# Optimization experiments

Hardware: AMD Instinct MI355X
Metric: run time of the kernel (lower is better)

## Reference

```python
import jax, jax.numpy as jnp
import numpy as np

DIM = 2048
N_HEADS = 16
HEAD_DIM = DIM // N_HEADS
ROPE_BASE = 10000


def l2norm(x, axis=-1, eps=1e-12):
    n = jnp.sqrt(jnp.sum(x * x, axis=axis, keepdims=True))
    return x / jnp.maximum(n, eps)


def rope_tables(T, dim, base, dtype):
    theta = 1.0 / (base ** (jnp.arange(0, dim, 2, dtype=dtype) / dim))  # [dim/2]
    ang = jnp.arange(T, dtype=dtype)[:, None] * theta[None, :]          # [T, dim/2]
    return jnp.sin(ang), jnp.cos(ang)


def apply_rope(x, sin, cos):
    # x: [B, H, T, D]; sin/cos: [T, D/2] (half-split convention, not interleaved)
    half = x.shape[-1] // 2
    xr, xi = x[..., :half], x[..., half:]
    yr = xr * cos - xi * sin
    yi = xr * sin + xi * cos
    return jnp.concatenate([yr, yi], axis=-1)


def setup_inputs() -> dict:
    key = jax.random.key(0)
    ks = jax.random.split(key, 5)
    B, T = 1, 2048
    x = jax.random.normal(ks[0], (B, T, DIM), dtype=jnp.float32)
    wq = jax.random.normal(ks[1], (DIM, DIM), dtype=jnp.float32) * 0.02
    wk = jax.random.normal(ks[2], (DIM, DIM), dtype=jnp.float32) * 0.02
    wv = jax.random.normal(ks[3], (DIM, DIM), dtype=jnp.float32) * 0.02
    wo = jax.random.normal(ks[4], (DIM, DIM), dtype=jnp.float32) * 0.02
    sqk = jnp.ones((N_HEADS, 1, HEAD_DIM), dtype=jnp.float32) * (1.0 / DIM ** 0.5)
    return {"x": x, "wq": wq, "wk": wk, "wv": wv, "wo": wo, "sqk": sqk}


def reference(x, wq, wk, wv, wo, sqk):
    B, T, C = x.shape
    H, D = N_HEADS, HEAD_DIM
    restore = C ** 0.5  # restore_scale_sqk = sqkinit / sqkscale
    actual_sqk = sqk * restore  # [H, 1, D]

    def proj(w):
        return jnp.einsum('btc,oc->bto', x, w).reshape(B, T, H, D).transpose(0, 2, 1, 3)

    q = proj(wq)  # [B, H, T, D]
    new_k = proj(wk)
    new_v = proj(wv)

    sin, cos = rope_tables(T, D, ROPE_BASE, x.dtype)
    q = apply_rope(q, sin, cos) * actual_sqk
    k = apply_rope(new_k, sin, cos) * actual_sqk

    # NOTE: original uses scale=head_dim**0.5 (multiplies by sqrt(D))
    scores = jnp.einsum('bhqd,bhkd->bhqk', q, k) * (D ** 0.5)
    mask = jnp.tril(jnp.ones((T, T), dtype=bool))
    scores = jnp.where(mask, scores, jnp.finfo(scores.dtype).min)
    attn = jax.nn.softmax(scores, axis=-1)
    out = jnp.einsum('bhqk,bhkd->bhqd', attn, new_v)  # [B, H, T, D]
    out = out.transpose(0, 2, 1, 3).reshape(B, T, C)
    out = jnp.einsum('btc,oc->bto', out, wo)
    return (l2norm(out), (new_k, new_v))
```

## Files before the change

kernel.cpp:

```cpp
#include <hip/hip_runtime.h>

typedef __bf16 bf16x8 __attribute__((ext_vector_type(8)));
typedef float f32x4 __attribute__((ext_vector_type(4)));
typedef unsigned short us4 __attribute__((ext_vector_type(4)));

constexpr int TT = 2048;
constexpr int CC = 2048;
constexpr int HH = 16;
constexpr int DD = 128;

__device__ __forceinline__ unsigned short f2bf(float f) {
  unsigned u = __builtin_bit_cast(unsigned, f);
  u += 0x7FFFu + ((u >> 16) & 1u);
  return (unsigned short)(u >> 16);
}
__device__ __forceinline__ float bf2f(unsigned short b) {
  unsigned u = ((unsigned)b) << 16;
  return __builtin_bit_cast(float, u);
}

__device__ __forceinline__ void gld_lds16(const unsigned short* g, unsigned short* l) {
  __builtin_amdgcn_global_load_lds(
      (const __attribute__((address_space(1))) unsigned int*)g,
      (__attribute__((address_space(3))) unsigned int*)l,
      16, 0, 0);
}

__device__ __forceinline__ int soff(int qt) {
  int g = qt >> 2, rem = qt & 3;
  return (g + 1) * (2 * g + rem);
}

__global__ __launch_bounds__(256) void k_f32_to_bf16(
    const float* __restrict__ src, unsigned short* __restrict__ dst, int n8) {
  int i = blockIdx.x * 256 + threadIdx.x;
  if (i >= n8) return;
  const float4* s = (const float4*)src;
  float4 a = s[2 * i], b = s[2 * i + 1];
  us4 lo = { f2bf(a.x), f2bf(a.y), f2bf(a.z), f2bf(a.w) };
  us4 hi = { f2bf(b.x), f2bf(b.y), f2bf(b.z), f2bf(b.w) };
  us4* d = (us4*)dst;
  d[2 * i] = lo;
  d[2 * i + 1] = hi;
}

template <int MODE>
__global__ __launch_bounds__(512, 2) void k_gemm256(
    const unsigned short* __restrict__ A, const unsigned short* __restrict__ B,
    int N, int K, int kspan,
    float* __restrict__ out0, float* __restrict__ out1,
    float* __restrict__ out2, float* __restrict__ out3) {
  __shared__ alignas(16) unsigned short As[2][2][128 * 64];
  __shared__ alignas(16) unsigned short Bs[2][2][128 * 64];
  const int tid = threadIdx.x;
  const int m0 = blockIdx.y * 256, n0 = blockIdx.x * 256;
  const int kbeg = blockIdx.z * kspan;
  const int NT = kspan >> 6;
  const int wid = tid >> 6, lane = tid & 63;
  const int wr = wid >> 2, wc = wid & 3;
  const int lr = lane & 15, lg = lane >> 4;
  const int swz = lr & 7;
  const int bh = wc >> 1;
  const int brow0 = (wc & 1) * 64;

  const int sr0 = tid >> 3, sc0 = tid & 7;
  const unsigned short* Ab = A + kbeg;
  const unsigned short* Bb = B + kbeg;

  auto stageA = [&](int buf, int half, int koff) {
#pragma unroll
    for (int j = 0; j < 2; ++j) {
      const int r = sr0 + j * 64;
      gld_lds16(Ab + (size_t)(m0 + half * 128 + r) * K + koff + ((sc0 ^ (r & 7)) * 8),
                &As[buf][half][(tid + j * 512) * 8]);
    }
  };
  auto stageB = [&](int buf, int half, int koff) {
#pragma unroll
    for (int j = 0; j < 2; ++j) {
      const int r = sr0 + j * 64;
      gld_lds16(Bb + (size_t)(n0 + half * 128 + r) * K + koff + ((sc0 ^ (r & 7)) * 8),
                &Bs[buf][half][(tid + j * 512) * 8]);
    }
  };

  f32x4 acc[8][4] = {};

  stageA(0, 0, 0); stageA(0, 1, 0); stageB(0, 0, 0); stageB(0, 1, 0);
  if (NT > 1) {
    stageA(1, 0, 64); stageA(1, 1, 64); stageB(1, 0, 64); stageB(1, 1, 64);
    asm volatile("s_waitcnt vmcnt(8)" ::: "memory");
  } else {
    asm volatile("s_waitcnt vmcnt(0)" ::: "memory");
  }
  __builtin_amdgcn_sched_barrier(0);
  __builtin_amdgcn_s_barrier();

  for (int t = 0; t < NT; ++t) {
    const int cur = t & 1;
    const int kN2 = (t + 2) * 64;
    const bool pf = (t + 2) < NT;
    bf16x8 alo[4][2], ahi[4][2], ba[2][2], bb[2][2];

#pragma unroll
    for (int im = 0; im < 4; ++im)
#pragma unroll
      for (int kk = 0; kk < 2; ++kk)
        alo[im][kk] = *(const bf16x8*)(&As[cur][wr][(im * 16 + lr) * 64 + (((kk * 4 + lg) ^ swz) * 8)]);
#pragma unroll
    for (int in = 0; in < 2; ++in)
#pragma unroll
      for (int kk = 0; kk < 2; ++kk)
        ba[in][kk] = *(const bf16x8*)(&Bs[cur][bh][(brow0 + in * 16 + lr) * 64 + (((kk * 4 + lg) ^ swz) * 8)]);
#pragma unroll
    for (int in = 0; in < 2; ++in)
#pragma unroll
      for (int kk = 0; kk < 2; ++kk)
        bb[in][kk] = *(const bf16x8*)(&Bs[cur][bh][(brow0 + (2 + in) * 16 + lr) * 64 + (((kk * 4 + lg) ^ swz) * 8)]);
    asm volatile("s_waitcnt lgkmcnt(4)" ::: "memory");
    __builtin_amdgcn_sched_barrier(0);

    __builtin_amdgcn_s_setprio(1);
#pragma unroll
    for (int im = 0; im < 4; ++im)
#pragma unroll
      for (int in = 0; in < 2; ++in)
#pragma unroll
        for (int kk = 0; kk < 2; ++kk)
          acc[im][in] = __builtin_amdgcn_mfma_f32_16x16x32_bf16(alo[im][kk], ba[in][kk], acc[im][in], 0, 0, 0);
    __builtin_amdgcn_s_setprio(0);
    asm volatile("s_waitcnt lgkmcnt(0)" ::: "memory");
    __builtin_amdgcn_sched_barrier(0);

    __builtin_amdgcn_s_setprio(1);
#pragma unroll
    for (int im = 0; im < 4; ++im)
#pragma unroll
      for (int in = 0; in < 2; ++in)
#pragma unroll
        for (int kk = 0; kk < 2; ++kk)
          acc[im][2 + in] = __builtin_amdgcn_mfma_f32_16x16x32_bf16(alo[im][kk], bb[in][kk], acc[im][2 + in], 0, 0, 0);
    __builtin_amdgcn_s_setprio(0);
    __builtin_amdgcn_sched_barrier(0);

#pragma unroll
    for (int im = 0; im < 4; ++im)
#pragma unroll
      for (int kk = 0; kk < 2; ++kk)
        ahi[im][kk] = *(const bf16x8*)(&As[cur][wr][((4 + im) * 16 + lr) * 64 + (((kk * 4 + lg) ^ swz) * 8)]);

    __builtin_amdgcn_s_barrier();
    if (pf) { stageB(cur, 0, kN2); stageB(cur, 1, kN2); }
    asm volatile("s_waitcnt lgkmcnt(0)" ::: "memory");
    __builtin_amdgcn_sched_barrier(0);

    __builtin_amdgcn_s_setprio(1);
#pragma unroll
    for (int im = 0; im < 4; ++im)
#pragma unroll
      for (int in = 0; in < 2; ++in)
#pragma unroll
        for (int kk = 0; kk < 2; ++kk)
          acc[4 + im][2 + in] = __builtin_amdgcn_mfma_f32_16x16x32_bf16(ahi[im][kk], bb[in][kk], acc[4 + im][2 + in], 0, 0, 0);
    __builtin_amdgcn_s_setprio(0);
    __builtin_amdgcn_sched_barrier(0);

    __builtin_amdgcn_s_barrier();
    if (pf) { stageA(cur, 0, kN2); stageA(cur, 1, kN2); }

    __builtin_amdgcn_s_setprio(1);
#pragma unroll
    for (int im = 0; im < 4; ++im)
#pragma unroll
      for (int in = 0; in < 2; ++in)
#pragma unroll
        for (int kk = 0; kk < 2; ++kk)
          acc[4 + im][in] = __builtin_amdgcn_mfma_f32_16x16x32_bf16(ahi[im][kk], ba[in][kk], acc[4 + im][in], 0, 0, 0);
    __builtin_amdgcn_s_setprio(0);
    __builtin_amdgcn_sched_barrier(0);
    if (pf) {
      asm volatile("s_waitcnt vmcnt(8)" ::: "memory");
    } else {
      asm volatile("s_waitcnt vmcnt(0)" ::: "memory");
    }
    __builtin_amdgcn_sched_barrier(0);
    __builtin_amdgcn_s_barrier();
  }

  float* dst = out0;
  if (MODE == 1) {
    int z = blockIdx.z;
    dst = (z == 0) ? out0 : (z == 1) ? out1 : (z == 2) ? out2 : out3;
  }
#pragma unroll
  for (int mf = 0; mf < 8; ++mf) {
    const int row = m0 + wr * 128 + mf * 16 + lg * 4;
#pragma unroll
    for (int nf = 0; nf < 4; ++nf) {
      const int col = n0 + wc * 64 + nf * 16 + lr;
#pragma unroll
      for (int r = 0; r < 4; ++r) {
        float v = acc[mf][nf][r];
        int rr = row + r;
        if (MODE == 0) {
          if (col < 2048) {
            out0[(size_t)rr * 2048 + col] = v;
          } else if (col < 4096) {
            int c = col - 2048;
            out1[(size_t)(c >> 7) * (TT * DD) + (size_t)rr * DD + (c & 127)] = v;
          } else {
            int c = col - 4096;
            out2[(size_t)(c >> 7) * (TT * DD) + (size_t)rr * DD + (c & 127)] = v;
          }
        } else {
          dst[(size_t)rr * N + col] = v;
        }
      }
    }
  }
}

__global__ __launch_bounds__(256) void k_rope(
    const float* __restrict__ Qf, const float* __restrict__ Kraw,
    const float* __restrict__ sqk,
    unsigned short* __restrict__ qb, unsigned short* __restrict__ kb) {
  const int t = blockIdx.x;
  for (int i = threadIdx.x; i < HH * 64; i += 256) {
    int h = i >> 6, dp = i & 63;
    float theta = expf(-(float)dp * 0.14391156831212787f);
    float ang = (float)t * theta;
    float sn, cs;
    sincosf(ang, &sn, &cs);
    float qr = Qf[(size_t)t * CC + h * DD + dp];
    float qi = Qf[(size_t)t * CC + h * DD + dp + 64];
    const float* kp = Kraw + (size_t)h * TT * DD + (size_t)t * DD;
    float kr = kp[dp], ki = kp[dp + 64];
    float sr = sqk[h * DD + dp];
    float si = sqk[h * DD + dp + 64];
    float qsr = sr * 512.0f, qsi = si * 512.0f;
    float ksr = sr * 45.25483399593904f, ksi = si * 45.25483399593904f;
    unsigned short* qo = qb + ((size_t)h * TT + t) * DD;
    unsigned short* ko = kb + ((size_t)h * TT + t) * DD;
    qo[dp]      = f2bf((qr * cs - qi * sn) * qsr);
    qo[dp + 64] = f2bf((qr * sn + qi * cs) * qsi);
    ko[dp]      = f2bf((kr * cs - ki * sn) * ksr);
    ko[dp + 64] = f2bf((kr * sn + ki * cs) * ksi);
  }
}

__global__ __launch_bounds__(256) void k_vt(
    const float* __restrict__ Vraw, unsigned short* __restrict__ vt) {
  const int h = blockIdx.z;
  const int t0 = blockIdx.x * 64, d0 = blockIdx.y * 64;
  __shared__ unsigned short tile[64][65];
  const float* vp = Vraw + (size_t)h * TT * DD;
  for (int i = threadIdx.x; i < 4096; i += 256) {
    int r = i >> 6, c = i & 63;
    tile[r][c] = f2bf(vp[(size_t)(t0 + r) * DD + d0 + c]);
  }
  __syncthreads();
  unsigned short* op = vt + (size_t)h * DD * TT;
  for (int i = threadIdx.x; i < 4096; i += 256) {
    int dr = i >> 6, tc = i & 63;
    op[(size_t)(d0 + dr) * TT + t0 + tc] = tile[tc][dr];
  }
}

__global__ __launch_bounds__(512) void k_attn_split(
    const unsigned short* __restrict__ qb, const unsigned short* __restrict__ kb,
    const unsigned short* __restrict__ vt,
    unsigned short* __restrict__ po, float* __restrict__ marr, float* __restrict__ larr) {
  const int qt = blockIdx.x, h = blockIdx.y, s = blockIdx.z;
  if (4 * s > qt) return;
  const int slot = h * 40 + soff(qt) + s;
  const int kbeg = 512 * s;
  const int kend = min(kbeg + 512, 128 * qt + 128);
  const int ntiles = (kend - kbeg) >> 6;
  const int tid = threadIdx.x;
  const int wid = tid >> 6, lane = tid & 63;
  const int lr = lane & 15, lg = lane >> 4;
  const int q0 = qt * 128 + wid * 16;

  __shared__ alignas(16) unsigned short Ks[64 * 128];
  __shared__ alignas(16) unsigned short Vs[128 * 64];
  __shared__ alignas(16) unsigned short P[8][16][72];

  const unsigned short* qh = qb + (size_t)h * TT * DD;
  const unsigned short* kh = kb + (size_t)h * TT * DD;
  const unsigned short* vh = vt + (size_t)h * DD * TT;

  bf16x8 qf[4];
#pragma unroll
  for (int c = 0; c < 4; ++c)
    qf[c] = *(const bf16x8*)(qh + (size_t)(q0 + lr) * DD + c * 32 + lg * 8);

  f32x4 acc[8] = {};
  float mrow[4] = {-3e38f, -3e38f, -3e38f, -3e38f};
  float lsum[4] = {0.f, 0.f, 0.f, 0.f};

  for (int kt = 0; kt < ntiles; ++kt) {
    const int k0 = kbeg + kt * 64;
#pragma unroll
    for (int half = 0; half < 2; ++half) {
      int ch = tid + half * 512;
      int r = ch >> 4, c4 = ch & 15;
      gld_lds16(kh + (size_t)(k0 + r) * DD + ((c4 ^ (r & 7)) * 8), Ks + ch * 8);
    }
#pragma unroll
    for (int half = 0; half < 2; ++half) {
      int ch = tid + half * 512;
      int d = ch >> 3, c8 = ch & 7;
      gld_lds16(vh + (size_t)d * TT + k0 + ((c8 ^ (d & 7)) * 8), Vs + ch * 8);
    }
    __syncthreads();

    if (k0 <= q0 + 15) {
      f32x4 sv[4] = {};
#pragma unroll
      for (int ktile = 0; ktile < 4; ++ktile) {
        const int row = ktile * 16 + lr;
#pragma unroll
        for (int c = 0; c < 4; ++c) {
          int chn = (c * 4 + lg) ^ (lr & 7);
          bf16x8 kf = *(const bf16x8*)(Ks + row * 128 + chn * 8);
          sv[ktile] = __builtin_amdgcn_mfma_f32_16x16x32_bf16(qf[c], kf, sv[ktile], 0, 0, 0);
        }
      }
      if (k0 + 63 > q0) {
#pragma unroll
        for (int ktile = 0; ktile < 4; ++ktile)
#pragma unroll
          for (int r = 0; r < 4; ++r) {
            int key = k0 + ktile * 16 + lr;
            int qrow = q0 + lg * 4 + r;
            if (key > qrow) sv[ktile][r] = -1e30f;
          }
      }
      float pmax[4];
#pragma unroll
      for (int r = 0; r < 4; ++r)
        pmax[r] = fmaxf(fmaxf(sv[0][r], sv[1][r]), fmaxf(sv[2][r], sv[3][r]));
#pragma unroll
      for (int msk = 1; msk <= 8; msk <<= 1)
#pragma unroll
        for (int r = 0; r < 4; ++r) pmax[r] = fmaxf(pmax[r], __shfl_xor(pmax[r], msk));
      float p[4][4], ps[4], scl[4];
#pragma unroll
      for (int r = 0; r < 4; ++r) {
        float mn = fmaxf(mrow[r], pmax[r]);
        scl[r] = __expf(mrow[r] - mn);
        mrow[r] = mn;
        ps[r] = 0.f;
#pragma unroll
        for (int ktile = 0; ktile < 4; ++ktile) {
          p[ktile][r] = __expf(sv[ktile][r] - mn);
          ps[r] += p[ktile][r];
        }
      }
#pragma unroll
      for (int msk = 1; msk <= 8; msk <<= 1)
#pragma unroll
        for (int r = 0; r < 4; ++r) ps[r] += __shfl_xor(ps[r], msk);
#pragma unroll
      for (int r = 0; r < 4; ++r) lsum[r] = lsum[r] * scl[r] + ps[r];
#pragma unroll
      for (int n = 0; n < 8; ++n)
#pragma unroll
        for (int r = 0; r < 4; ++r) acc[n][r] *= scl[r];
#pragma unroll
      for (int ktile = 0; ktile < 4; ++ktile)
#pragma unroll
        for (int r = 0; r < 4; ++r)
          P[wid][lg * 4 + r][ktile * 16 + lr] = f2bf(p[ktile][r]);
      asm volatile("s_waitcnt lgkmcnt(0)" ::: "memory");
      __builtin_amdgcn_sched_barrier(0);
      bf16x8 pf[2];
#pragma unroll
      for (int ks = 0; ks < 2; ++ks)
        pf[ks] = *(const bf16x8*)(&P[wid][lr][ks * 32 + lg * 8]);
#pragma unroll
      for (int n = 0; n < 8; ++n) {
        const int row = n * 16 + lr;
#pragma unroll
        for (int ks = 0; ks < 2; ++ks) {
          int chn = (ks * 4 + lg) ^ (lr & 7);
          bf16x8 vf = *(const bf16x8*)(Vs + row * 64 + chn * 8);
          acc[n] = __builtin_amdgcn_mfma_f32_16x16x32_bf16(pf[ks], vf, acc[n], 0, 0, 0);
        }
      }
    }
    __syncthreads();
  }

  unsigned short* pob = po + (size_t)slot * (128 * DD);
#pragma unroll
  for (int n = 0; n < 8; ++n)
#pragma unroll
    for (int r = 0; r < 4; ++r) {
      int row = wid * 16 + lg * 4 + r;
      pob[(size_t)row * DD + n * 16 + lr] = f2bf(acc[n][r]);
    }
  if (lr == 0) {
#pragma unroll
    for (int r = 0; r < 4; ++r) {
      int row = wid * 16 + lg * 4 + r;
      marr[(size_t)slot * 128 + row] = mrow[r];
      larr[(size_t)slot * 128 + row] = lsum[r];
    }
  }
}

__global__ __launch_bounds__(256) void k_attn_reduce(
    const unsigned short* __restrict__ po, const float* __restrict__ marr,
    const float* __restrict__ larr, unsigned short* __restrict__ ob) {
  const int qt = blockIdx.x, h = blockIdx.y;
  const int ns = (qt >> 2) + 1;
  const int sb = h * 40 + soff(qt);
  const int tid = threadIdx.x;
  const int row = tid >> 1, d0 = (tid & 1) * 64;
  float mstar = -3e38f;
  for (int s = 0; s < ns; ++s) mstar = fmaxf(mstar, marr[(size_t)(sb + s) * 128 + row]);
  float w[4];
  float ltot = 0.f;
  for (int s = 0; s < ns; ++s) {
    w[s] = __expf(marr[(size_t)(sb + s) * 128 + row] - mstar);
    ltot += w[s] * larr[(size_t)(sb + s) * 128 + row];
  }
  float inv = 1.0f / ltot;
  float o[64] = {};
  for (int s = 0; s < ns; ++s) {
    const bf16x8* pp = (const bf16x8*)(po + (size_t)(sb + s) * (128 * DD) + (size_t)row * DD + d0);
    float ws = w[s];
#pragma unroll
    for (int j = 0; j < 8; ++j) {
      bf16x8 v = pp[j];
#pragma unroll
      for (int e = 0; e < 8; ++e) o[j * 8 + e] += ws * (float)v[e];
    }
  }
  unsigned short* op = ob + (size_t)(qt * 128 + row) * CC + h * DD + d0;
#pragma unroll
  for (int j = 0; j < 16; ++j) {
    us4 t = { f2bf(o[4 * j] * inv), f2bf(o[4 * j + 1] * inv),
              f2bf(o[4 * j + 2] * inv), f2bf(o[4 * j + 3] * inv) };
    ((us4*)op)[j] = t;
  }
}

__global__ __launch_bounds__(256) void k_l2norm(
    const float* __restrict__ Of0, const float* __restrict__ Of1,
    const float* __restrict__ Of2, const float* __restrict__ Of3,
    float* __restrict__ out) {
  const int t = blockIdx.x;
  const int tid = threadIdx.x;
  const float4* p0 = (const float4*)(Of0 + (size_t)t * CC);
  const float4* p1 = (const float4*)(Of1 + (size_t)t * CC);
  const float4* p2 = (const float4*)(Of2 + (size_t)t * CC);
  const float4* p3 = (const float4*)(Of3 + (size_t)t * CC);
  float4 a = p0[2 * tid], b = p0[2 * tid + 1];
  float4 a1 = p1[2 * tid], b1 = p1[2 * tid + 1];
  float4 a2 = p2[2 * tid], b2 = p2[2 * tid + 1];
  float4 a3 = p3[2 * tid], b3 = p3[2 * tid + 1];
  a.x += a1.x + a2.x + a3.x; a.y += a1.y + a2.y + a3.y;
  a.z += a1.z + a2.z + a3.z; a.w += a1.w + a2.w + a3.w;
  b.x += b1.x + b2.x + b3.x; b.y += b1.y + b2.y + b3.y;
  b.z += b1.z + b2.z + b3.z; b.w += b1.w + b2.w + b3.w;
  float ss = a.x * a.x + a.y * a.y + a.z * a.z + a.w * a.w +
             b.x * b.x + b.y * b.y + b.z * b.z + b.w * b.w;
#pragma unroll
  for (int msk = 1; msk < 64; msk <<= 1) ss += __shfl_xor(ss, msk);
  __shared__ float red[4];
  if ((tid & 63) == 0) red[tid >> 6] = ss;
  __syncthreads();
  ss = red[0] + red[1] + red[2] + red[3];
  float sc = 1.0f / fmaxf(sqrtf(ss), 1e-12f);
  float4 oa = { a.x * sc, a.y * sc, a.z * sc, a.w * sc };
  float4 obv = { b.x * sc, b.y * sc, b.z * sc, b.w * sc };
  float4* o = (float4*)(out + (size_t)t * CC);
  o[2 * tid] = oa;
  o[2 * tid + 1] = obv;
}

extern "C" void kernel_launch(void* const* d_in, const int* in_sizes, int n_in,
                              void* d_out, int out_size, void* d_ws, size_t ws_size,
                              hipStream_t stream) {
  const float* x   = (const float*)d_in[0];
  const float* wq  = (const float*)d_in[1];
  const float* wk  = (const float*)d_in[2];
  const float* wv  = (const float*)d_in[3];
  const float* wo  = (const float*)d_in[4];
  const float* sqk = (const float*)d_in[5];

  float* out_norm = (float*)d_out;
  float* out_k = out_norm + (size_t)4 * 1024 * 1024;
  float* out_v = out_norm + (size_t)8 * 1024 * 1024;

  char* ws = (char*)d_ws;
  unsigned short* xb  = (unsigned short*)(ws);
  unsigned short* w1b = (unsigned short*)(ws + (8u << 20));
  unsigned short* wob = (unsigned short*)(ws + (32u << 20));
  unsigned short* qb  = (unsigned short*)(ws + (40u << 20));
  unsigned short* kb  = (unsigned short*)(ws + (48u << 20));
  unsigned short* vtb = (unsigned short*)(ws + (56u << 20));
  unsigned short* obb = (unsigned short*)(ws + (64u << 20));
  float* Qf = (float*)(ws + (72u << 20));

  unsigned short* po = (unsigned short*)(ws);
  float* marr = (float*)(ws + (22u << 20));
  float* larr = (float*)(ws + (23u << 20));

  float* Of0 = Qf;
  float* Of1 = (float*)(ws);
  float* Of2 = (float*)(ws + (16u << 20));
  float* Of3 = (float*)(ws + (40u << 20));

  const int n8 = (CC * CC) / 8;
  k_f32_to_bf16<<<n8 / 256, 256, 0, stream>>>(x,  xb, n8);
  k_f32_to_bf16<<<n8 / 256, 256, 0, stream>>>(wq, w1b, n8);
  k_f32_to_bf16<<<n8 / 256, 256, 0, stream>>>(wk, w1b + (size_t)4 * 1024 * 1024, n8);
  k_f32_to_bf16<<<n8 / 256, 256, 0, stream>>>(wv, w1b + (size_t)8 * 1024 * 1024, n8);
  k_f32_to_bf16<<<n8 / 256, 256, 0, stream>>>(wo, wob, n8);

  k_gemm256<0><<<dim3(24, 8, 1), 512, 0, stream>>>(xb, w1b, 3 * CC, CC, CC,
                                                   Qf, out_k, out_v, nullptr);

  k_rope<<<TT, 256, 0, stream>>>(Qf, out_k, sqk, qb, kb);
  k_vt<<<dim3(32, 2, 16), 256, 0, stream>>>(out_v, vtb);

  k_attn_split<<<dim3(16, 16, 4), 512, 0, stream>>>(qb, kb, vtb, po, marr, larr);
  k_attn_reduce<<<dim3(16, 16), 256, 0, stream>>>(po, marr, larr, obb);

  k_gemm256<1><<<dim3(8, 8, 4), 512, 0, stream>>>(obb, wob, CC, CC, CC / 4,
                                                  Of0, Of1, Of2, Of3);

  k_l2norm<<<TT, 256, 0, stream>>>(Of0, Of1, Of2, Of3, out_norm);
}
```

Measured before the change: 226.9 us.

## Restructure GEMM pipeline into 8-phase schedule and fuse five conversion launches

```diff
diff --git a/kernel.cpp b/kernel.cpp
--- a/kernel.cpp
+++ b/kernel.cpp
@@ -31,10 +31,17 @@
   return (g + 1) * (2 * g + rem);
 }
 
-__global__ __launch_bounds__(256) void k_f32_to_bf16(
-    const float* __restrict__ src, unsigned short* __restrict__ dst, int n8) {
+__global__ __launch_bounds__(256) void k_cvt5(
+    const float* __restrict__ s0, const float* __restrict__ s1,
+    const float* __restrict__ s2, const float* __restrict__ s3,
+    const float* __restrict__ s4,
+    unsigned short* __restrict__ d0, unsigned short* __restrict__ d1,
+    unsigned short* __restrict__ d2, unsigned short* __restrict__ d3,
+    unsigned short* __restrict__ d4) {
+  const int m = blockIdx.y;
+  const float* src = (m == 0) ? s0 : (m == 1) ? s1 : (m == 2) ? s2 : (m == 3) ? s3 : s4;
+  unsigned short* dst = (m == 0) ? d0 : (m == 1) ? d1 : (m == 2) ? d2 : (m == 3) ? d3 : d4;
   int i = blockIdx.x * 256 + threadIdx.x;
-  if (i >= n8) return;
   const float4* s = (const float4*)src;
   float4 a = s[2 * i], b = s[2 * i + 1];
   us4 lo = { f2bf(a.x), f2bf(a.y), f2bf(a.z), f2bf(a.w) };
@@ -45,7 +52,7 @@
 }
 
 template <int MODE>
-__global__ __launch_bounds__(512, 2) void k_gemm256(
+__global__ __launch_bounds__(512, 2) void k_gemm8p(
     const unsigned short* __restrict__ A, const unsigned short* __restrict__ B,
     int N, int K, int kspan,
     float* __restrict__ out0, float* __restrict__ out1,
@@ -55,19 +62,18 @@
   const int tid = threadIdx.x;
   const int m0 = blockIdx.y * 256, n0 = blockIdx.x * 256;
   const int kbeg = blockIdx.z * kspan;
-  const int NT = kspan >> 6;
+  const int NT = kspan >> 6, NT2 = NT >> 1;
   const int wid = tid >> 6, lane = tid & 63;
   const int wr = wid >> 2, wc = wid & 3;
   const int lr = lane & 15, lg = lane >> 4;
-  const int swz = lr & 7;
-  const int bh = wc >> 1;
-  const int brow0 = (wc & 1) * 64;
+  const int bh = wc >> 1, brow0 = (wc & 1) * 64;
 
   const int sr0 = tid >> 3, sc0 = tid & 7;
   const unsigned short* Ab = A + kbeg;
   const unsigned short* Bb = B + kbeg;
 
-  auto stageA = [&](int buf, int half, int koff) {
+  auto stageA = [&](int buf, int half, int tile) {
+    const int koff = tile * 64;
 #pragma unroll
     for (int j = 0; j < 2; ++j) {
       const int r = sr0 + j * 64;
@@ -75,7 +81,8 @@
                 &As[buf][half][(tid + j * 512) * 8]);
     }
   };
-  auto stageB = [&](int buf, int half, int koff) {
+  auto stageB = [&](int buf, int half, int tile) {
+    const int koff = tile * 64;
 #pragma unroll
     for (int j = 0; j < 2; ++j) {
       const int r = sr0 + j * 64;
@@ -85,107 +92,122 @@
   };
 
   f32x4 acc[8][4] = {};
-
-  stageA(0, 0, 0); stageA(0, 1, 0); stageB(0, 0, 0); stageB(0, 1, 0);
-  if (NT > 1) {
-    stageA(1, 0, 64); stageA(1, 1, 64); stageB(1, 0, 64); stageB(1, 1, 64);
-    asm volatile("s_waitcnt vmcnt(8)" ::: "memory");
-  } else {
-    asm volatile("s_waitcnt vmcnt(0)" ::: "memory");
-  }
+  bf16x8 alo[4][2], ahi[4][2], ba[2][2], bb[2][2];
+
+  auto rdAlo = [&](int d) {
+#pragma unroll
+    for (int im = 0; im < 4; ++im)
+#pragma unroll
+      for (int kk = 0; kk < 2; ++kk) {
+        const int row = im * 16 + lr;
+        alo[im][kk] = *(const bf16x8*)(&As[d][wr][row * 64 + (((kk * 4 + lg) ^ (row & 7)) * 8)]);
+      }
+  };
+  auto rdAhi = [&](int d) {
+#pragma unroll
+    for (int im = 0; im < 4; ++im)
+#pragma unroll
+      for (int kk = 0; kk < 2; ++kk) {
+        const int row = (4 + im) * 16 + lr;
+        ahi[im][kk] = *(const bf16x8*)(&As[d][wr][row * 64 + (((kk * 4 + lg) ^ (row & 7)) * 8)]);
+      }
+  };
+  auto rdBa = [&](int d) {
+#pragma unroll
+    for (int in = 0; in < 2; ++in)
+#pragma unroll
+      for (int kk = 0; kk < 2; ++kk) {
+        const int row = brow0 + in * 16 + lr;
+        ba[in][kk] = *(const bf16x8*)(&Bs[d][bh][row * 64 + (((kk * 4 + lg) ^ (row & 7)) * 8)]);
+      }
+  };
+  auto rdBb = [&](int d) {
+#pragma unroll
+    for (int in = 0; in < 2; ++in)
+#pragma unroll
+      for (int kk = 0; kk < 2; ++kk) {
+        const int row = brow0 + (2 + in) * 16 + lr;
+        bb[in][kk] = *(const bf16x8*)(&Bs[d][bh][row * 64 + (((kk * 4 + lg) ^ (row & 7)) * 8)]);
+      }
+  };
+
+#define MFMA_Q(MB, NB, AF, BF)                                                     \
+  __builtin_amdgcn_s_setprio(1);                                                   \
+  _Pragma("unroll") for (int im = 0; im < 4; ++im)                                 \
+      _Pragma("unroll") for (int in = 0; in < 2; ++in)                             \
+          _Pragma("unroll") for (int kk = 0; kk < 2; ++kk)                         \
+              acc[MB + im][NB + in] = __builtin_amdgcn_mfma_f32_16x16x32_bf16(     \
+                  AF[im][kk], BF[in][kk], acc[MB + im][NB + in], 0, 0, 0);         \
+  __builtin_amdgcn_s_setprio(0);
+
+#define WAIT_LGKM0                                      \
+  asm volatile("s_waitcnt lgkmcnt(0)" ::: "memory");    \
   __builtin_amdgcn_sched_barrier(0);
-  __builtin_amdgcn_s_barrier();
-
-  for (int t = 0; t < NT; ++t) {
-    const int cur = t & 1;
-    const int kN2 = (t + 2) * 64;
-    const bool pf = (t + 2) < NT;
-    bf16x8 alo[4][2], ahi[4][2], ba[2][2], bb[2][2];
-
-#pragma unroll
-    for (int im = 0; im < 4; ++im)
-#pragma unroll
-      for (int kk = 0; kk < 2; ++kk)
-        alo[im][kk] = *(const bf16x8*)(&As[cur][wr][(im * 16 + lr) * 64 + (((kk * 4 + lg) ^ swz) * 8)]);
-#pragma unroll
-    for (int in = 0; in < 2; ++in)
-#pragma unroll
-      for (int kk = 0; kk < 2; ++kk)
-        ba[in][kk] = *(const bf16x8*)(&Bs[cur][bh][(brow0 + in * 16 + lr) * 64 + (((kk * 4 + lg) ^ swz) * 8)]);
-#pragma unroll
-    for (int in = 0; in < 2; ++in)
-#pragma unroll
-      for (int kk = 0; kk < 2; ++kk)
-        bb[in][kk] = *(const bf16x8*)(&Bs[cur][bh][(brow0 + (2 + in) * 16 + lr) * 64 + (((kk * 4 + lg) ^ swz) * 8)]);
-    asm volatile("s_waitcnt lgkmcnt(4)" ::: "memory");
+#define BAR __builtin_amdgcn_s_barrier();
+
+  stageB(0, 0, 0); stageB(0, 1, 0); stageA(0, 0, 0); stageA(0, 1, 0);
+  if (NT > 1) { stageB(1, 0, 1); stageB(1, 1, 1); }
+  asm volatile("s_waitcnt vmcnt(4)" ::: "memory");
+  __builtin_amdgcn_sched_barrier(0);
+  BAR
+
+  for (int t = 0; t < NT2; ++t) {
+    const int t1 = 2 * t + 1, t2 = 2 * t + 2, t3 = 2 * t + 3;
+    const bool s2 = t2 < NT, s3 = t3 < NT;
+
+    rdAlo(0); rdBa(0);
+    stageA(1, 0, t1);
+    BAR WAIT_LGKM0
+    MFMA_Q(0, 0, alo, ba)
+    BAR
+
+    rdBb(0);
+    stageA(1, 1, t1);
+    BAR WAIT_LGKM0
+    MFMA_Q(0, 2, alo, bb)
+    BAR
+
+    rdAhi(0);
+    if (s2) stageB(0, 0, t2);
+    BAR WAIT_LGKM0
+    MFMA_Q(4, 2, ahi, bb)
+    BAR
+
+    if (s2) stageB(0, 1, t2);
+    MFMA_Q(4, 0, ahi, ba)
+    if (s2) { asm volatile("s_waitcnt vmcnt(4)" ::: "memory"); }
+    else    { asm volatile("s_waitcnt vmcnt(0)" ::: "memory"); }
     __builtin_amdgcn_sched_barrier(0);
-
-    __builtin_amdgcn_s_setprio(1);
-#pragma unroll
-    for (int im = 0; im < 4; ++im)
-#pragma unroll
-      for (int in = 0; in < 2; ++in)
-#pragma unroll
-        for (int kk = 0; kk < 2; ++kk)
-          acc[im][in] = __builtin_amdgcn_mfma_f32_16x16x32_bf16(alo[im][kk], ba[in][kk], acc[im][in], 0, 0, 0);
-    __builtin_amdgcn_s_setprio(0);
-    asm volatile("s_waitcnt lgkmcnt(0)" ::: "memory");
+    BAR
+
+    rdAlo(1); rdBa(1);
+    if (s2) stageA(0, 0, t2);
+    BAR WAIT_LGKM0
+    MFMA_Q(0, 0, alo, ba)
+    BAR
+
+    rdBb(1);
+    if (s2) stageA(0, 1, t2);
+    BAR WAIT_LGKM0
+    MFMA_Q(0, 2, alo, bb)
+    BAR
+
+    rdAhi(1);
+    if (s3) stageB(1, 0, t3);
+    BAR WAIT_LGKM0
+    MFMA_Q(4, 2, ahi, bb)
+    BAR
+
+    if (s3) stageB(1, 1, t3);
+    MFMA_Q(4, 0, ahi, ba)
+    if (s3) { asm volatile("s_waitcnt vmcnt(4)" ::: "memory"); }
+    else    { asm volatile("s_waitcnt vmcnt(0)" ::: "memory"); }
     __builtin_amdgcn_sched_barrier(0);
-
-    __builtin_amdgcn_s_setprio(1);
-#pragma unroll
-    for (int im = 0; im < 4; ++im)
-#pragma unroll
-      for (int in = 0; in < 2; ++in)
-#pragma unroll
-        for (int kk = 0; kk < 2; ++kk)
-          acc[im][2 + in] = __builtin_amdgcn_mfma_f32_16x16x32_bf16(alo[im][kk], bb[in][kk], acc[im][2 + in], 0, 0, 0);
-    __builtin_amdgcn_s_setprio(0);
-    __builtin_amdgcn_sched_barrier(0);
-
-#pragma unroll
-    for (int im = 0; im < 4; ++im)
-#pragma unroll
-      for (int kk = 0; kk < 2; ++kk)
-        ahi[im][kk] = *(const bf16x8*)(&As[cur][wr][((4 + im) * 16 + lr) * 64 + (((kk * 4 + lg) ^ swz) * 8)]);
-
-    __builtin_amdgcn_s_barrier();
-    if (pf) { stageB(cur, 0, kN2); stageB(cur, 1, kN2); }
-    asm volatile("s_waitcnt lgkmcnt(0)" ::: "memory");
-    __builtin_amdgcn_sched_barrier(0);
-
-    __builtin_amdgcn_s_setprio(1);
-#pragma unroll
-    for (int im = 0; im < 4; ++im)
-#pragma unroll
-      for (int in = 0; in < 2; ++in)
-#pragma unroll
-        for (int kk = 0; kk < 2; ++kk)
-          acc[4 + im][2 + in] = __builtin_amdgcn_mfma_f32_16x16x32_bf16(ahi[im][kk], bb[in][kk], acc[4 + im][2 + in], 0, 0, 0);
-    __builtin_amdgcn_s_setprio(0);
-    __builtin_amdgcn_sched_barrier(0);
-
-    __builtin_amdgcn_s_barrier();
-    if (pf) { stageA(cur, 0, kN2); stageA(cur, 1, kN2); }
-
-    __builtin_amdgcn_s_setprio(1);
-#pragma unroll
-    for (int im = 0; im < 4; ++im)
-#pragma unroll
-      for (int in = 0; in < 2; ++in)
-#pragma unroll
-        for (int kk = 0; kk < 2; ++kk)
-          acc[4 + im][in] = __builtin_amdgcn_mfma_f32_16x16x32_bf16(ahi[im][kk], ba[in][kk], acc[4 + im][in], 0, 0, 0);
-    __builtin_amdgcn_s_setprio(0);
-    __builtin_amdgcn_sched_barrier(0);
-    if (pf) {
-      asm volatile("s_waitcnt vmcnt(8)" ::: "memory");
-    } else {
-      asm volatile("s_waitcnt vmcnt(0)" ::: "memory");
-    }
-    __builtin_amdgcn_sched_barrier(0);
-    __builtin_amdgcn_s_barrier();
-  }
+    BAR
+  }
+#undef MFMA_Q
+#undef WAIT_LGKM0
+#undef BAR
 
   float* dst = out0;
   if (MODE == 1) {
@@ -514,15 +536,12 @@
   float* Of2 = (float*)(ws + (16u << 20));
   float* Of3 = (float*)(ws + (40u << 20));
 
-  const int n8 = (CC * CC) / 8;
-  k_f32_to_bf16<<<n8 / 256, 256, 0, stream>>>(x,  xb, n8);
-  k_f32_to_bf16<<<n8 / 256, 256, 0, stream>>>(wq, w1b, n8);
-  k_f32_to_bf16<<<n8 / 256, 256, 0, stream>>>(wk, w1b + (size_t)4 * 1024 * 1024, n8);
-  k_f32_to_bf16<<<n8 / 256, 256, 0, stream>>>(wv, w1b + (size_t)8 * 1024 * 1024, n8);
-  k_f32_to_bf16<<<n8 / 256, 256, 0, stream>>>(wo, wob, n8);
-
-  k_gemm256<0><<<dim3(24, 8, 1), 512, 0, stream>>>(xb, w1b, 3 * CC, CC, CC,
-                                                   Qf, out_k, out_v, nullptr);
+  k_cvt5<<<dim3(2048, 5), 256, 0, stream>>>(
+      x, wq, wk, wv, wo,
+      xb, w1b, w1b + (size_t)4 * 1024 * 1024, w1b + (size_t)8 * 1024 * 1024, wob);
+
+  k_gemm8p<0><<<dim3(24, 8, 1), 512, 0, stream>>>(xb, w1b, 3 * CC, CC, CC,
+                                                  Qf, out_k, out_v, nullptr);
 
   k_rope<<<TT, 256, 0, stream>>>(Qf, out_k, sqk, qb, kb);
   k_vt<<<dim3(32, 2, 16), 256, 0, stream>>>(out_v, vtb);
@@ -530,8 +549,8 @@
   k_attn_split<<<dim3(16, 16, 4), 512, 0, stream>>>(qb, kb, vtb, po, marr, larr);
   k_attn_reduce<<<dim3(16, 16), 256, 0, stream>>>(po, marr, larr, obb);
 
-  k_gemm256<1><<<dim3(8, 8, 4), 512, 0, stream>>>(obb, wob, CC, CC, CC / 4,
-                                                  Of0, Of1, Of2, Of3);
+  k_gemm8p<1><<<dim3(8, 8, 4), 512, 0, stream>>>(obb, wob, CC, CC, CC / 4,
+                                                 Of0, Of1, Of2, Of3);
 
   k_l2norm<<<TT, 256, 0, stream>>>(Of0, Of1, Of2, Of3, out_norm);
 }
```

Measured after the change: 223.4 us. Within noise of the previous version (-1.5%).
